# Kernel tuning notes

Hardware: AMD Instinct MI355X
Metric: run time of the kernel (lower is better)

Reference implementation:

```python
import jax, jax.numpy as jnp
import numpy as np

# --- MLA config (DeepSeek-V3 style, scaled) ---
HIDDEN = 4096
N_HEADS = 32
Q_LORA = 1536
KV_LORA = 512
ROPE_D = 64
NOPE_D = 128
V_D = 128
Q_HEAD_D = NOPE_D + ROPE_D  # 192
EPS = 1e-6
SCALING = Q_HEAD_D ** (-0.5)
ROPE_THETA = 10000.0
B, S = 1, 2048


def rms_norm(x, w):
    var = jnp.mean(jnp.square(x.astype(jnp.float32)), axis=-1, keepdims=True)
    return (x * jax.lax.rsqrt(var + EPS)).astype(x.dtype) * w


def rotate_half(x):
    x1, x2 = jnp.split(x, 2, axis=-1)
    return jnp.concatenate([-x2, x1], axis=-1)


def apply_rope(x, cos, sin):
    # x: [B, H, S, ROPE_D]; cos/sin: [B, S, ROPE_D] -> unsqueeze head dim
    c = cos[:, None, :, :]
    s = sin[:, None, :, :]
    return x * c + rotate_half(x) * s


def setup_inputs() -> dict:
    key = jax.random.key(0)
    ks = jax.random.split(key, 8)
    hidden_states = jax.random.normal(ks[0], (B, S, HIDDEN), dtype=jnp.float32)
    # real RoPE tables
    inv_freq = 1.0 / (ROPE_THETA ** (np.arange(0, ROPE_D, 2, dtype=np.float32) / ROPE_D))
    t = np.arange(S, dtype=np.float32)
    freqs = np.outer(t, inv_freq)                      # [S, ROPE_D/2]
    emb = np.concatenate([freqs, freqs], axis=-1)      # [S, ROPE_D]
    cos = jnp.asarray(np.cos(emb))[None].repeat(B, 0)  # [B, S, ROPE_D]
    sin = jnp.asarray(np.sin(emb))[None].repeat(B, 0)
    scale = lambda fan_in: 1.0 / np.sqrt(fan_in)
    w_q_a = jax.random.normal(ks[1], (Q_LORA, HIDDEN), dtype=jnp.float32) * scale(HIDDEN)
    q_a_ln_w = jnp.ones((Q_LORA,), dtype=jnp.float32)
    w_q_b = jax.random.normal(ks[2], (N_HEADS * Q_HEAD_D, Q_LORA), dtype=jnp.float32) * scale(Q_LORA)
    w_kv_a = jax.random.normal(ks[3], (KV_LORA + ROPE_D, HIDDEN), dtype=jnp.float32) * scale(HIDDEN)
    kv_a_ln_w = jnp.ones((KV_LORA,), dtype=jnp.float32)
    w_kv_b = jax.random.normal(ks[4], (N_HEADS * (NOPE_D + V_D), KV_LORA), dtype=jnp.float32) * scale(KV_LORA)
    w_o = jax.random.normal(ks[5], (HIDDEN, N_HEADS * V_D), dtype=jnp.float32) * scale(N_HEADS * V_D)
    return {
        'hidden_states': hidden_states, 'cos': cos, 'sin': sin,
        'w_q_a': w_q_a, 'q_a_ln_w': q_a_ln_w, 'w_q_b': w_q_b,
        'w_kv_a': w_kv_a, 'kv_a_ln_w': kv_a_ln_w, 'w_kv_b': w_kv_b, 'w_o': w_o,
    }


def reference(hidden_states, cos, sin, w_q_a, q_a_ln_w, w_q_b, w_kv_a, kv_a_ln_w, w_kv_b, w_o):
    b, s, _ = hidden_states.shape
    # --- Q path: low-rank down + RMSNorm + up ---
    q_lat = rms_norm(hidden_states @ w_q_a.T, q_a_ln_w)              # [B,S,Q_LORA]
    q = (q_lat @ w_q_b.T).reshape(b, s, N_HEADS, Q_HEAD_D)
    q = q.transpose(0, 2, 1, 3)                                       # [B,H,S,Q_HEAD_D]
    q_nope, q_rot = q[..., :NOPE_D], q[..., NOPE_D:]                  # (note: source names swapped)
    # --- KV path: shared compressed latent + single rotary key ---
    ckv = hidden_states @ w_kv_a.T                                    # [B,S,KV_LORA+ROPE_D]
    k_lat, k_rot = ckv[..., :KV_LORA], ckv[..., KV_LORA:]
    kv = (rms_norm(k_lat, kv_a_ln_w) @ w_kv_b.T).reshape(b, s, N_HEADS, NOPE_D + V_D)
    kv = kv.transpose(0, 2, 1, 3)                                     # [B,H,S,NOPE_D+V_D]
    k_nope, v = kv[..., :NOPE_D], kv[..., NOPE_D:]
    k_rot = k_rot.reshape(b, 1, s, ROPE_D)                            # single rotary key head
    # --- partial RoPE on rotary slices ---
    q_rot = apply_rope(q_rot, cos, sin)
    k_rot = apply_rope(k_rot, cos, sin)
    k_rot = jnp.broadcast_to(k_rot, (b, N_HEADS, s, ROPE_D))
    query = jnp.concatenate([q_rot, q_nope], axis=-1)                 # [B,H,S,192]
    key = jnp.concatenate([k_rot, k_nope], axis=-1)                   # [B,H,S,192]
    # --- eager causal attention ---
    scores = jnp.einsum('bhqd,bhkd->bhqk', query, key) * SCALING
    causal = jnp.tril(jnp.ones((s, s), dtype=bool))
    scores = jnp.where(causal[None, None], scores, jnp.finfo(scores.dtype).min)
    probs = jax.nn.softmax(scores, axis=-1)
    attn = jnp.einsum('bhqk,bhkd->bhqd', probs, v)                    # [B,H,S,V_D]
    attn = attn.transpose(0, 2, 1, 3).reshape(b, s, N_HEADS * V_D)
    return attn @ w_o.T                                               # [B,S,HIDDEN]
```

## Files before the change

kernel.cpp:

```cpp
#include <hip/hip_runtime.h>

typedef unsigned short u16;
typedef u16 u16x4 __attribute__((ext_vector_type(4)));
typedef u16 u16x8 __attribute__((ext_vector_type(8)));
typedef float f32x4 __attribute__((ext_vector_type(4)));
typedef __bf16 bf16x8 __attribute__((ext_vector_type(8)));

#define S_LEN 2048
#define HIDDEN_D 4096
#define NHEADS 32
#define QLORA 1536
#define KVLORA 512
#define ROPED 64
#define NOPED 128
#define VDIM 128
#define QHD 192
#define SCALING_F 0.07216878364870323f

__device__ __forceinline__ u16 f2bf(float x) {
  union { float f; unsigned u; } v; v.f = x;
  unsigned r = v.u + 0x7fffu + ((v.u >> 16) & 1u);
  return (u16)(r >> 16);
}
__device__ __forceinline__ float bf2f(u16 x) {
  union { unsigned u; float f; } v; v.u = ((unsigned)x) << 16; return v.f;
}

__device__ __forceinline__ f32x4 mfma_bf16(u16x8 a, u16x8 b, f32x4 c) {
  return __builtin_amdgcn_mfma_f32_16x16x32_bf16(
      __builtin_bit_cast(bf16x8, a), __builtin_bit_cast(bf16x8, b), c, 0, 0, 0);
}

__global__ __launch_bounds__(256) void cvt_all(
    const float* __restrict__ hsrc, u16* __restrict__ Hb,
    const float* __restrict__ wqa, const float* __restrict__ wkva, u16* __restrict__ WqaKva,
    const float* __restrict__ wkvb, u16* __restrict__ Wkvb,
    const float* __restrict__ wo, u16* __restrict__ Wo)
{
  const int b = blockIdx.x, t = threadIdx.x;
  const float* src; u16* dst; size_t idx;
  if (b < 8192)       { src = hsrc; dst = Hb;     idx = (size_t)b * 256 + t; }
  else if (b < 14336) { src = wqa;  dst = WqaKva; idx = (size_t)(b - 8192) * 256 + t; }
  else if (b < 16640) { src = wkva; dst = WqaKva + (size_t)QLORA * HIDDEN_D; idx = (size_t)(b - 14336) * 256 + t; }
  else if (b < 20736) { src = wkvb; dst = Wkvb;   idx = (size_t)(b - 16640) * 256 + t; }
  else                { src = wo;   dst = Wo;     idx = (size_t)(b - 20736) * 256 + t; }
  f32x4 v = ((const f32x4*)src)[idx];
  u16x4 o;
  o[0] = f2bf(v[0]); o[1] = f2bf(v[1]); o[2] = f2bf(v[2]); o[3] = f2bf(v[3]);
  ((u16x4*)dst)[idx] = o;
}

__global__ __launch_bounds__(256) void cvt_qperm(const float* __restrict__ in,
                                                 u16* __restrict__ out) {
  const size_t idx = (size_t)blockIdx.x * 256 + threadIdx.x;
  const int row = (int)(idx / 384), c4 = (int)(idx % 384);
  const int h = row / 192, d = row - h * 192;
  const int newd = (d >= 128) ? (d - 128) : (d + 64);
  f32x4 v = ((const f32x4*)in)[idx];
  u16x4 o;
  o[0] = f2bf(v[0]); o[1] = f2bf(v[1]); o[2] = f2bf(v[2]); o[3] = f2bf(v[3]);
  ((u16x4*)out)[(size_t)(h * 192 + newd) * 384 + c4] = o;
}


#define GEMM_PROLOGUE(BIDX)                                                    \
  __shared__ u16 sA[2][128 * 64];                                              \
  __shared__ u16 sB[2][128 * 64];                                              \
  const int tid = threadIdx.x;                                                 \
  const int wid = tid >> 6, lane = tid & 63;                                   \
  const int lr = lane & 15, lg = lane >> 4;                                    \
  const int nbn = (N + 127) >> 7;                                              \
  const int bx = (BIDX) % nbn, by = (BIDX) / nbn;                              \
  const int bm = by << 7, bn = bx << 7;                                        \
  const int wm = (wid >> 1) << 6, wn = (wid & 1) << 6;                         \
  const int kbase = blockIdx.y * Ks;                                           \
  f32x4 acc[4][4] = {};                                                        \
  u16x8 areg[4], breg[4];                                                      \
  auto loadA = [&](int k0) {                                                   \
    _Pragma("unroll")                                                          \
    for (int i = 0; i < 4; ++i) {                                              \
      int chunk = i * 256 + tid;                                               \
      int row = chunk >> 3, c8 = chunk & 7;                                    \
      int gr = bm + row; if (gr >= M) gr = M - 1;                              \
      areg[i] = *(const u16x8*)(A + (size_t)gr * lda + k0 + (c8 << 3));        \
    }                                                                          \
  };                                                                           \
  auto loadB = [&](int k0) {                                                   \
    _Pragma("unroll")                                                          \
    for (int i = 0; i < 4; ++i) {                                              \
      int chunk = i * 256 + tid;                                               \
      int n = chunk >> 3, c8 = chunk & 7;                                      \
      int gn = bn + n; if (gn >= N) gn = N - 1;                                \
      breg[i] = *(const u16x8*)(B + (size_t)gn * ldb + k0 + (c8 << 3));        \
    }                                                                          \
  };                                                                           \
  auto writeAB = [&](int buf) {                                                \
    _Pragma("unroll")                                                          \
    for (int i = 0; i < 4; ++i) {                                              \
      *(u16x8*)&sA[buf][(i * 256 + tid) * 8] = areg[i];                        \
      *(u16x8*)&sB[buf][(i * 256 + tid) * 8] = breg[i];                        \
    }                                                                          \
  };                                                                           \
  auto compute = [&](int buf) {                                                \
    const u16* pa = sA[buf];                                                   \
    const u16* pb = sB[buf];                                                   \
    _Pragma("unroll")                                                          \
    for (int ks = 0; ks < 2; ++ks) {                                           \
      const int kof = ks * 32 + lg * 8;                                        \
      u16x8 av[4], bv[4];                                                      \
      _Pragma("unroll")                                                        \
      for (int m = 0; m < 4; ++m) av[m] = *(const u16x8*)&pa[(wm + m * 16 + lr) * 64 + kof]; \
      _Pragma("unroll")                                                        \
      for (int n = 0; n < 4; ++n) bv[n] = *(const u16x8*)&pb[(wn + n * 16 + lr) * 64 + kof]; \
      _Pragma("unroll")                                                        \
      for (int m = 0; m < 4; ++m)                                              \
        _Pragma("unroll")                                                      \
        for (int n = 0; n < 4; ++n)                                            \
          acc[m][n] = mfma_bf16(av[m], bv[n], acc[m][n]);                      \
    }                                                                          \
  };                                                                           \
  const int nk = Ks >> 6;                                                      \
  loadA(kbase); loadB(kbase);                                                  \
  writeAB(0);                                                                  \
  __syncthreads();                                                             \
  for (int t = 0; t < nk; ++t) {                                               \
    const int cur = t & 1;                                                     \
    if (t + 1 < nk) { loadA(kbase + ((t + 1) << 6)); loadB(kbase + ((t + 1) << 6)); } \
    compute(cur);                                                              \
    if (t + 1 < nk) { writeAB(cur ^ 1); }                                      \
    __syncthreads();                                                           \
  }

__global__ __launch_bounds__(256, 2) void gemm_ff(
    const u16* __restrict__ A, const u16* __restrict__ B, float* __restrict__ C,
    int M, int N, int Ks, int lda, int ldb, int ldc)
{
  C += (size_t)blockIdx.y * M * ldc;
  GEMM_PROLOGUE(blockIdx.x)
#pragma unroll
  for (int m = 0; m < 4; ++m) {
    const int row0 = bm + wm + m * 16 + (lg << 2);
#pragma unroll
    for (int n = 0; n < 4; ++n) {
      const int col = bn + wn + n * 16 + lr;
      if (col < N) {
#pragma unroll
        for (int r = 0; r < 4; ++r)
          C[(size_t)(row0 + r) * ldc + col] = acc[m][n][r];
      }
    }
  }
}

__global__ __launch_bounds__(256, 2) void gemm_qb_kvb(
    const u16* __restrict__ qlatn, const u16* __restrict__ Wqb,
    const float* __restrict__ cosp, const float* __restrict__ sinp, u16* __restrict__ Qb,
    const u16* __restrict__ klatn, const u16* __restrict__ Wkvb,
    u16* __restrict__ Knope, u16* __restrict__ Vt)
{
  if (blockIdx.x < 768) {
    const u16* A = qlatn; const u16* B = Wqb;
    const int M = 2048, N = 6144, Ks = 1536, lda = 1536, ldb = 1536;
    GEMM_PROLOGUE(blockIdx.x)
#pragma unroll
    for (int m = 0; m < 4; ++m) {
      const int row0 = bm + wm + m * 16 + (lg << 2);
#pragma unroll
      for (int n = 0; n < 2; ++n) {
        const int col = bn + wn + n * 16 + lr;
        const int h = col / 192, tc = col - h * 192;
        if (tc < 32) {
#pragma unroll
          for (int r = 0; r < 4; ++r) {
            const int s = row0 + r;
            const float cx = cosp[s * 64 + tc],      sx = sinp[s * 64 + tc];
            const float cy = cosp[s * 64 + tc + 32], sy = sinp[s * 64 + tc + 32];
            const float xv = acc[m][n][r], yv = acc[m][n + 2][r];
            Qb[((size_t)h * 2048 + s) * QHD + tc]      = f2bf((xv * cx - yv * sx) * SCALING_F);
            Qb[((size_t)h * 2048 + s) * QHD + tc + 32] = f2bf((yv * cy + xv * sy) * SCALING_F);
          }
        }
      }
#pragma unroll
      for (int n = 0; n < 4; ++n) {
        const int col = bn + wn + n * 16 + lr;
        const int h = col / 192, tc = col - h * 192;
        if (tc >= 64) {
#pragma unroll
          for (int r = 0; r < 4; ++r) {
            const int s = row0 + r;
            Qb[((size_t)h * 2048 + s) * QHD + tc] = f2bf(acc[m][n][r] * SCALING_F);
          }
        }
      }
    }
  } else {
    const u16* A = klatn; const u16* B = Wkvb;
    const int M = 2048, N = 8192, Ks = 512, lda = 512, ldb = 512;
    GEMM_PROLOGUE(blockIdx.x - 768)
#pragma unroll
    for (int m = 0; m < 4; ++m) {
      const int row0 = bm + wm + m * 16 + (lg << 2);
#pragma unroll
      for (int n = 0; n < 4; ++n) {
        const int col = bn + wn + n * 16 + lr;
        const int h = col >> 8, c = col & 255;
        if (c < 128) {
#pragma unroll
          for (int r = 0; r < 4; ++r)
            Knope[((size_t)h * 2048 + row0 + r) * 128 + c] = f2bf(acc[m][n][r]);
        } else {
          u16x4 v;
          v[0] = f2bf(acc[m][n][0]); v[1] = f2bf(acc[m][n][1]);
          v[2] = f2bf(acc[m][n][2]); v[3] = f2bf(acc[m][n][3]);
          *(u16x4*)&Vt[((size_t)h * 128 + (c - 128)) * 2048 + row0] = v;
        }
      }
    }
  }
}

__global__ __launch_bounds__(256) void norm_fused(
    const float* __restrict__ qkv_part,
    const float* __restrict__ q_a_ln, const float* __restrict__ kv_a_ln,
    const float* __restrict__ cosp, const float* __restrict__ sinp,
    u16* __restrict__ qlatn, u16* __restrict__ klatn, u16* __restrict__ krot)
{
  const size_t PSTRIDE = (size_t)S_LEN * 2112;
  __shared__ float sb[4];
  if (blockIdx.x < 2048) {
    const int row = blockIdx.x;
    const float* x = qkv_part + (size_t)row * 2112;
    float ss = 0.f;
    for (int i = threadIdx.x * 4; i < 1536; i += 1024) {
      f32x4 v = *(const f32x4*)&x[i];
      f32x4 v2 = *(const f32x4*)&x[PSTRIDE + i];
      v[0] += v2[0]; v[1] += v2[1]; v[2] += v2[2]; v[3] += v2[3];
      ss += v[0] * v[0] + v[1] * v[1] + v[2] * v[2] + v[3] * v[3];
    }
#pragma unroll
    for (int off = 32; off >= 1; off >>= 1) ss += __shfl_xor(ss, off, 64);
    if ((threadIdx.x & 63) == 0) sb[threadIdx.x >> 6] = ss;
    __syncthreads();
    const float inv = rsqrtf((sb[0] + sb[1] + sb[2] + sb[3]) / 1536.0f + 1e-6f);
    u16* o = qlatn + (size_t)row * 1536;
    for (int i = threadIdx.x * 4; i < 1536; i += 1024) {
      f32x4 v = *(const f32x4*)&x[i];
      f32x4 v2 = *(const f32x4*)&x[PSTRIDE + i];
      v[0] += v2[0]; v[1] += v2[1]; v[2] += v2[2]; v[3] += v2[3];
      f32x4 wv = *(const f32x4*)&q_a_ln[i];
      u16x4 u;
      u[0] = f2bf(v[0] * inv * wv[0]); u[1] = f2bf(v[1] * inv * wv[1]);
      u[2] = f2bf(v[2] * inv * wv[2]); u[3] = f2bf(v[3] * inv * wv[3]);
      *(u16x4*)&o[i] = u;
    }
  } else {
    const int s = blockIdx.x - 2048;
    const float* x = qkv_part + 1536 + (size_t)s * 2112;
    const int i2 = threadIdx.x * 2;
    float a = x[i2] + x[PSTRIDE + i2];
    float b = x[i2 + 1] + x[PSTRIDE + i2 + 1];
    float ss = a * a + b * b;
#pragma unroll
    for (int off = 32; off >= 1; off >>= 1) ss += __shfl_xor(ss, off, 64);
    if ((threadIdx.x & 63) == 0) sb[threadIdx.x >> 6] = ss;
    __syncthreads();
    const float inv = rsqrtf((sb[0] + sb[1] + sb[2] + sb[3]) / 512.0f + 1e-6f);
    klatn[(size_t)s * 512 + i2]     = f2bf(a * inv * kv_a_ln[i2]);
    klatn[(size_t)s * 512 + i2 + 1] = f2bf(b * inv * kv_a_ln[i2 + 1]);
    if (threadIdx.x < 64) {
      const int d = threadIdx.x;
      const float xr = x[512 + d] + x[PSTRIDE + 512 + d];
      const int dp = (d < 32) ? (d + 32) : (d - 32);
      const float rrabs = x[512 + dp] + x[PSTRIDE + 512 + dp];
      const float rr = (d < 32) ? -rrabs : rrabs;
      krot[(size_t)s * 64 + d] = f2bf(xr * cosp[s * 64 + d] + rr * sinp[s * 64 + d]);
    }
  }
}

__global__ __launch_bounds__(256, 2) void flash_kernel(
    const u16* __restrict__ Qb, const u16* __restrict__ Krot,
    const u16* __restrict__ Knope, const u16* __restrict__ Vt,
    u16* __restrict__ attnb)
{
  const int h = blockIdx.x & 31, qt = blockIdx.x >> 5;
  const int q0 = qt << 7;
  __shared__ u16 sK[64][QHD];
  __shared__ u16 sV[VDIM][64];
  __shared__ u16 sP[4][32][64];
  const int tid = threadIdx.x;
  const int wid = tid >> 6, lane = tid & 63;
  const int lr = lane & 15, lg = lane >> 4;

  u16x8 qf[2][6];
#pragma unroll
  for (int m = 0; m < 2; ++m) {
    const int row = q0 + wid * 32 + m * 16 + lr;
#pragma unroll
    for (int kk = 0; kk < 6; ++kk)
      qf[m][kk] = *(const u16x8*)&Qb[((size_t)h * 2048 + row) * QHD + kk * 32 + lg * 8];
  }

  f32x4 acc[2][8] = {};
  float mx[2][4], ls[2][4];
#pragma unroll
  for (int m = 0; m < 2; ++m)
#pragma unroll
    for (int r = 0; r < 4; ++r) { mx[m][r] = -1e30f; ls[m][r] = 0.f; }

  const int nkv = q0 + 128;
  u16x8 kreg[6], vreg[4];

  auto loadKV = [&](int kv0) {
#pragma unroll
    for (int i = 0; i < 6; ++i) {
      const int chunk = i * 256 + tid;
      const int row = chunk / 24, cc = chunk % 24;
      const u16* src = (cc < 8)
          ? &Krot[(size_t)(kv0 + row) * 64 + cc * 8]
          : &Knope[((size_t)h * 2048 + kv0 + row) * 128 + (cc - 8) * 8];
      kreg[i] = *(const u16x8*)src;
    }
#pragma unroll
    for (int i = 0; i < 4; ++i) {
      const int chunk = i * 256 + tid;
      const int d = chunk >> 3, c = chunk & 7;
      vreg[i] = *(const u16x8*)&Vt[((size_t)h * VDIM + d) * 2048 + kv0 + c * 8];
    }
  };

  loadKV(0);
  for (int kv0 = 0; kv0 < nkv; kv0 += 64) {
    __syncthreads();
    u16* kbase = &sK[0][0];
#pragma unroll
    for (int i = 0; i < 6; ++i) *(u16x8*)&kbase[(size_t)(i * 256 + tid) * 8] = kreg[i];
    u16* vbase = &sV[0][0];
#pragma unroll
    for (int i = 0; i < 4; ++i) *(u16x8*)&vbase[(size_t)(i * 256 + tid) * 8] = vreg[i];
    __syncthreads();
    if (kv0 + 64 < nkv) loadKV(kv0 + 64);

    f32x4 sc[2][4] = {};
#pragma unroll
    for (int kk = 0; kk < 6; ++kk) {
      u16x8 bfr[4];
#pragma unroll
      for (int n = 0; n < 4; ++n) bfr[n] = *(const u16x8*)&sK[n * 16 + lr][kk * 32 + lg * 8];
#pragma unroll
      for (int m = 0; m < 2; ++m)
#pragma unroll
        for (int n = 0; n < 4; ++n)
          sc[m][n] = mfma_bf16(qf[m][kk], bfr[n], sc[m][n]);
    }

    if (kv0 + 63 > q0 + wid * 32) {
#pragma unroll
      for (int m = 0; m < 2; ++m)
#pragma unroll
        for (int n = 0; n < 4; ++n) {
          const int kv = kv0 + n * 16 + lr;
#pragma unroll
          for (int r = 0; r < 4; ++r) {
            const int rowq = q0 + wid * 32 + m * 16 + lg * 4 + r;
            if (kv > rowq) sc[m][n][r] = -1e30f;
          }
        }
    }

#pragma unroll
    for (int m = 0; m < 2; ++m) {
      float rs[4];
#pragma unroll
      for (int r = 0; r < 4; ++r) {
        float v = fmaxf(fmaxf(sc[m][0][r], sc[m][1][r]), fmaxf(sc[m][2][r], sc[m][3][r]));
#pragma unroll
        for (int off = 1; off < 16; off <<= 1) v = fmaxf(v, __shfl_xor(v, off, 64));
        const float mnew = fmaxf(mx[m][r], v);
        const float alpha = __expf(mx[m][r] - mnew);
        mx[m][r] = mnew;
        ls[m][r] *= alpha;
#pragma unroll
        for (int df = 0; df < 8; ++df) acc[m][df][r] *= alpha;
        rs[r] = 0.f;
      }
#pragma unroll
      for (int n = 0; n < 4; ++n)
#pragma unroll
        for (int r = 0; r < 4; ++r) {
          const float p = __expf(sc[m][n][r] - mx[m][r]);
          rs[r] += p;
          sP[wid][m * 16 + lg * 4 + r][n * 16 + lr] = f2bf(p);
        }
#pragma unroll
      for (int r = 0; r < 4; ++r) {
        float v = rs[r];
#pragma unroll
        for (int off = 1; off < 16; off <<= 1) v += __shfl_xor(v, off, 64);
        ls[m][r] += v;
      }
    }

#pragma unroll
    for (int ks = 0; ks < 2; ++ks) {
      u16x8 pf0 = *(const u16x8*)&sP[wid][lr][ks * 32 + lg * 8];
      u16x8 pf1 = *(const u16x8*)&sP[wid][16 + lr][ks * 32 + lg * 8];
#pragma unroll
      for (int df = 0; df < 8; ++df) {
        u16x8 vf = *(const u16x8*)&sV[df * 16 + lr][ks * 32 + lg * 8];
        acc[0][df] = mfma_bf16(pf0, vf, acc[0][df]);
        acc[1][df] = mfma_bf16(pf1, vf, acc[1][df]);
      }
    }
  }

#pragma unroll
  for (int m = 0; m < 2; ++m)
#pragma unroll
    for (int df = 0; df < 8; ++df) {
      const int col = h * 128 + df * 16 + lr;
#pragma unroll
      for (int r = 0; r < 4; ++r) {
        const int row = q0 + wid * 32 + m * 16 + lg * 4 + r;
        attnb[(size_t)row * 4096 + col] = f2bf(acc[m][df][r] / ls[m][r]);
      }
    }
}

extern "C" void kernel_launch(void* const* d_in, const int* in_sizes, int n_in,
                              void* d_out, int out_size, void* d_ws, size_t ws_size,
                              hipStream_t stream) {
  (void)in_sizes; (void)n_in; (void)out_size; (void)ws_size;
  const float* hidden  = (const float*)d_in[0];
  const float* cosp    = (const float*)d_in[1];
  const float* sinp    = (const float*)d_in[2];
  const float* w_q_a   = (const float*)d_in[3];
  const float* q_a_ln  = (const float*)d_in[4];
  const float* w_q_b   = (const float*)d_in[5];
  const float* w_kv_a  = (const float*)d_in[6];
  const float* kv_a_ln = (const float*)d_in[7];
  const float* w_kv_b  = (const float*)d_in[8];
  const float* w_o     = (const float*)d_in[9];
  float* out = (float*)d_out;

  char* p = (char*)d_ws;
  auto alloc = [&](size_t bytes) { char* r = p; p += (bytes + 255) & ~(size_t)255; return r; };
  u16* Hb      = (u16*)alloc((size_t)S_LEN * HIDDEN_D * 2);
  u16* qlatn   = (u16*)alloc((size_t)S_LEN * QLORA * 2);
  u16* klatn   = (u16*)alloc((size_t)S_LEN * KVLORA * 2);
  u16* krot    = (u16*)alloc((size_t)S_LEN * ROPED * 2);
  u16* Qb      = (u16*)alloc((size_t)NHEADS * S_LEN * QHD * 2);
  u16* Knope   = (u16*)alloc((size_t)NHEADS * S_LEN * NOPED * 2);
  u16* Vt      = (u16*)alloc((size_t)NHEADS * VDIM * S_LEN * 2);
  u16* attnb   = (u16*)alloc((size_t)S_LEN * 4096 * 2);
  u16* WqaKva  = (u16*)alloc((size_t)2112 * HIDDEN_D * 2);
  u16* Wqb     = (u16*)alloc((size_t)6144 * QLORA * 2);
  u16* Wkvb    = (u16*)alloc((size_t)8192 * KVLORA * 2);
  u16* Wo      = (u16*)alloc((size_t)HIDDEN_D * 4096 * 2);
  float* qkv_part = (float*)alloc((size_t)2 * S_LEN * 2112 * 4);

  cvt_all<<<37120, 256, 0, stream>>>(hidden, Hb, w_q_a, w_kv_a, WqaKva, w_kv_b, Wkvb, w_o, Wo);
  cvt_qperm<<<9216, 256, 0, stream>>>(w_q_b, Wqb);
  gemm_ff<<<dim3(16 * 17, 2), 256, 0, stream>>>(Hb, WqaKva, qkv_part, 2048, 2112, 2048, 4096, 4096, 2112);
  norm_fused<<<4096, 256, 0, stream>>>(qkv_part, q_a_ln, kv_a_ln, cosp, sinp, qlatn, klatn, krot);
  gemm_qb_kvb<<<768 + 1024, 256, 0, stream>>>(qlatn, Wqb, cosp, sinp, Qb, klatn, Wkvb, Knope, Vt);
  flash_kernel<<<512, 256, 0, stream>>>(Qb, krot, Knope, Vt, attnb);
  gemm_ff<<<dim3(16 * 32, 1), 256, 0, stream>>>(attnb, Wo, out, 2048, 4096, 4096, 4096, 4096, 4096);
}
```

Measured before the change: 608.9 us.

## Split fused q_b/kv_b GEMM into separate kernels with standalone RoPE epilogue

```diff
diff --git a/kernel.cpp b/kernel.cpp
--- a/kernel.cpp
+++ b/kernel.cpp
@@ -50,27 +50,25 @@
   ((u16x4*)dst)[idx] = o;
 }
 
-__global__ __launch_bounds__(256) void cvt_qperm(const float* __restrict__ in,
-                                                 u16* __restrict__ out) {
-  const size_t idx = (size_t)blockIdx.x * 256 + threadIdx.x;
-  const int row = (int)(idx / 384), c4 = (int)(idx % 384);
-  const int h = row / 192, d = row - h * 192;
-  const int newd = (d >= 128) ? (d - 128) : (d + 64);
-  f32x4 v = ((const f32x4*)in)[idx];
+__global__ __launch_bounds__(256) void cvt_kernel(const float* __restrict__ in,
+                                                  u16* __restrict__ out, int n4) {
+  int i = blockIdx.x * 256 + threadIdx.x;
+  if (i >= n4) return;
+  f32x4 v = ((const f32x4*)in)[i];
   u16x4 o;
   o[0] = f2bf(v[0]); o[1] = f2bf(v[1]); o[2] = f2bf(v[2]); o[3] = f2bf(v[3]);
-  ((u16x4*)out)[(size_t)(h * 192 + newd) * 384 + c4] = o;
-}
-
-
-#define GEMM_PROLOGUE(BIDX)                                                    \
+  ((u16x4*)out)[i] = o;
+}
+
+
+#define GEMM_PROLOGUE()                                                        \
   __shared__ u16 sA[2][128 * 64];                                              \
   __shared__ u16 sB[2][128 * 64];                                              \
   const int tid = threadIdx.x;                                                 \
   const int wid = tid >> 6, lane = tid & 63;                                   \
   const int lr = lane & 15, lg = lane >> 4;                                    \
   const int nbn = (N + 127) >> 7;                                              \
-  const int bx = (BIDX) % nbn, by = (BIDX) / nbn;                              \
+  const int bx = blockIdx.x % nbn, by = blockIdx.x / nbn;                      \
   const int bm = by << 7, bn = bx << 7;                                        \
   const int wm = (wid >> 1) << 6, wn = (wid & 1) << 6;                         \
   const int kbase = blockIdx.y * Ks;                                           \
@@ -136,7 +134,7 @@
     int M, int N, int Ks, int lda, int ldb, int ldc)
 {
   C += (size_t)blockIdx.y * M * ldc;
-  GEMM_PROLOGUE(blockIdx.x)
+  GEMM_PROLOGUE()
 #pragma unroll
   for (int m = 0; m < 4; ++m) {
     const int row0 = bm + wm + m * 16 + (lg << 2);
@@ -152,69 +150,46 @@
   }
 }
 
-__global__ __launch_bounds__(256, 2) void gemm_qb_kvb(
-    const u16* __restrict__ qlatn, const u16* __restrict__ Wqb,
-    const float* __restrict__ cosp, const float* __restrict__ sinp, u16* __restrict__ Qb,
-    const u16* __restrict__ klatn, const u16* __restrict__ Wkvb,
-    u16* __restrict__ Knope, u16* __restrict__ Vt)
-{
-  if (blockIdx.x < 768) {
-    const u16* A = qlatn; const u16* B = Wqb;
-    const int M = 2048, N = 6144, Ks = 1536, lda = 1536, ldb = 1536;
-    GEMM_PROLOGUE(blockIdx.x)
-#pragma unroll
-    for (int m = 0; m < 4; ++m) {
-      const int row0 = bm + wm + m * 16 + (lg << 2);
-#pragma unroll
-      for (int n = 0; n < 2; ++n) {
-        const int col = bn + wn + n * 16 + lr;
-        const int h = col / 192, tc = col - h * 192;
-        if (tc < 32) {
-#pragma unroll
-          for (int r = 0; r < 4; ++r) {
-            const int s = row0 + r;
-            const float cx = cosp[s * 64 + tc],      sx = sinp[s * 64 + tc];
-            const float cy = cosp[s * 64 + tc + 32], sy = sinp[s * 64 + tc + 32];
-            const float xv = acc[m][n][r], yv = acc[m][n + 2][r];
-            Qb[((size_t)h * 2048 + s) * QHD + tc]      = f2bf((xv * cx - yv * sx) * SCALING_F);
-            Qb[((size_t)h * 2048 + s) * QHD + tc + 32] = f2bf((yv * cy + xv * sy) * SCALING_F);
-          }
-        }
-      }
-#pragma unroll
-      for (int n = 0; n < 4; ++n) {
-        const int col = bn + wn + n * 16 + lr;
-        const int h = col / 192, tc = col - h * 192;
-        if (tc >= 64) {
-#pragma unroll
-          for (int r = 0; r < 4; ++r) {
-            const int s = row0 + r;
-            Qb[((size_t)h * 2048 + s) * QHD + tc] = f2bf(acc[m][n][r] * SCALING_F);
-          }
-        }
-      }
-    }
-  } else {
-    const u16* A = klatn; const u16* B = Wkvb;
-    const int M = 2048, N = 8192, Ks = 512, lda = 512, ldb = 512;
-    GEMM_PROLOGUE(blockIdx.x - 768)
-#pragma unroll
-    for (int m = 0; m < 4; ++m) {
-      const int row0 = bm + wm + m * 16 + (lg << 2);
-#pragma unroll
-      for (int n = 0; n < 4; ++n) {
-        const int col = bn + wn + n * 16 + lr;
-        const int h = col >> 8, c = col & 255;
-        if (c < 128) {
-#pragma unroll
-          for (int r = 0; r < 4; ++r)
-            Knope[((size_t)h * 2048 + row0 + r) * 128 + c] = f2bf(acc[m][n][r]);
-        } else {
-          u16x4 v;
-          v[0] = f2bf(acc[m][n][0]); v[1] = f2bf(acc[m][n][1]);
-          v[2] = f2bf(acc[m][n][2]); v[3] = f2bf(acc[m][n][3]);
-          *(u16x4*)&Vt[((size_t)h * 128 + (c - 128)) * 2048 + row0] = v;
-        }
+__global__ __launch_bounds__(256, 2) void gemm_fb(
+    const u16* __restrict__ A, const u16* __restrict__ B, u16* __restrict__ C,
+    int M, int N, int Ks, int lda, int ldb, int ldc)
+{
+  GEMM_PROLOGUE()
+#pragma unroll
+  for (int m = 0; m < 4; ++m) {
+    const int row0 = bm + wm + m * 16 + (lg << 2);
+#pragma unroll
+    for (int n = 0; n < 4; ++n) {
+      const int col = bn + wn + n * 16 + lr;
+#pragma unroll
+      for (int r = 0; r < 4; ++r)
+        C[(size_t)(row0 + r) * ldc + col] = f2bf(acc[m][n][r]);
+    }
+  }
+}
+
+__global__ __launch_bounds__(256, 2) void gemm_kvb(
+    const u16* __restrict__ A, const u16* __restrict__ B,
+    u16* __restrict__ Knope, u16* __restrict__ Vt,
+    int M, int N, int Ks, int lda, int ldb)
+{
+  GEMM_PROLOGUE()
+#pragma unroll
+  for (int m = 0; m < 4; ++m) {
+    const int row0 = bm + wm + m * 16 + (lg << 2);
+#pragma unroll
+    for (int n = 0; n < 4; ++n) {
+      const int col = bn + wn + n * 16 + lr;
+      const int h = col >> 8, c = col & 255;
+      if (c < 128) {
+#pragma unroll
+        for (int r = 0; r < 4; ++r)
+          Knope[((size_t)h * 2048 + row0 + r) * 128 + c] = f2bf(acc[m][n][r]);
+      } else {
+        u16x4 v;
+        v[0] = f2bf(acc[m][n][0]); v[1] = f2bf(acc[m][n][1]);
+        v[2] = f2bf(acc[m][n][2]); v[3] = f2bf(acc[m][n][3]);
+        *(u16x4*)&Vt[((size_t)h * 128 + (c - 128)) * 2048 + row0] = v;
       }
     }
   }
@@ -276,6 +251,24 @@
       const float rr = (d < 32) ? -rrabs : rrabs;
       krot[(size_t)s * 64 + d] = f2bf(xr * cosp[s * 64 + d] + rr * sinp[s * 64 + d]);
     }
+  }
+}
+
+__global__ __launch_bounds__(256) void q_epi_kernel(const u16* __restrict__ q_raw,
+    const float* __restrict__ cosp, const float* __restrict__ sinp, u16* __restrict__ Qb) {
+  const int s = blockIdx.x;
+  const u16* x = q_raw + (size_t)s * 6144;
+  for (int idx = threadIdx.x; idx < 6144; idx += 256) {
+    const int h = idx / 192, d = idx - h * 192;
+    float v;
+    if (d < 64) {
+      const float xr = bf2f(x[h * 192 + 128 + d]);
+      const float rr = (d < 32) ? -bf2f(x[h * 192 + 160 + d]) : bf2f(x[h * 192 + 96 + d]);
+      v = xr * cosp[s * 64 + d] + rr * sinp[s * 64 + d];
+    } else {
+      v = bf2f(x[h * 192 + d - 64]);
+    }
+    Qb[((size_t)h * 2048 + s) * QHD + d] = f2bf(v * SCALING_F);
   }
 }
 
@@ -458,13 +451,16 @@
   u16* Wqb     = (u16*)alloc((size_t)6144 * QLORA * 2);
   u16* Wkvb    = (u16*)alloc((size_t)8192 * KVLORA * 2);
   u16* Wo      = (u16*)alloc((size_t)HIDDEN_D * 4096 * 2);
+  u16* qraw16  = (u16*)alloc((size_t)S_LEN * 6144 * 2);
   float* qkv_part = (float*)alloc((size_t)2 * S_LEN * 2112 * 4);
 
   cvt_all<<<37120, 256, 0, stream>>>(hidden, Hb, w_q_a, w_kv_a, WqaKva, w_kv_b, Wkvb, w_o, Wo);
-  cvt_qperm<<<9216, 256, 0, stream>>>(w_q_b, Wqb);
+  cvt_kernel<<<(6144 * QLORA / 4 + 255) / 256, 256, 0, stream>>>(w_q_b, Wqb, 6144 * QLORA / 4);
   gemm_ff<<<dim3(16 * 17, 2), 256, 0, stream>>>(Hb, WqaKva, qkv_part, 2048, 2112, 2048, 4096, 4096, 2112);
   norm_fused<<<4096, 256, 0, stream>>>(qkv_part, q_a_ln, kv_a_ln, cosp, sinp, qlatn, klatn, krot);
-  gemm_qb_kvb<<<768 + 1024, 256, 0, stream>>>(qlatn, Wqb, cosp, sinp, Qb, klatn, Wkvb, Knope, Vt);
+  gemm_fb<<<dim3(16 * 48, 1), 256, 0, stream>>>(qlatn, Wqb, qraw16, 2048, 6144, 1536, 1536, 1536, 6144);
+  q_epi_kernel<<<2048, 256, 0, stream>>>(qraw16, cosp, sinp, Qb);
+  gemm_kvb<<<dim3(16 * 64, 1), 256, 0, stream>>>(klatn, Wkvb, Knope, Vt, 2048, 8192, 512, 512, 512);
   flash_kernel<<<512, 256, 0, stream>>>(Qb, krot, Knope, Vt, attnb);
   gemm_ff<<<dim3(16 * 32, 1), 256, 0, stream>>>(attnb, Wo, out, 2048, 4096, 4096, 4096, 4096, 4096);
 }
```

Measured after the change: 586.0 us. 3.8% less time.
